# Kernel optimization log

Measured on AMD Instinct MI355X. Metric: run time of the kernel, lower is better.

## Reference

```python
import jax, jax.numpy as jnp
import numpy as np
jax.config.update("jax_enable_x64", True)
from jax.scipy.special import i0e

P = 256            # feature_num / contrast_dim
C = 1000           # num_classes
N = 512            # batch
TEMPERATURE = 1.0
ORDER = P // 2 - 1 # Bessel order nu = p/2 - 1


def _normalize(x, axis=-1, eps=1e-12):
    n = jnp.linalg.norm(x, axis=axis, keepdims=True)
    return x / jnp.maximum(n, eps)


def miller_recurrence(order, kappa):
    """Vectorized Miller backward recurrence for log I_order(k), log I_{order+1}(k).
    kappa: float64 array of any shape. Returns (log_I_order_scaled, log_I_order1_scaled)
    matching the torch reference (exponentially-scaled via i0e)."""
    ones = jnp.ones(kappa.shape, jnp.float64)
    zeros = jnp.zeros(kappa.shape, jnp.float64)
    init = (ones, zeros, zeros, zeros, zeros, zeros, zeros)
    iis = jnp.arange(2 * order, 0, -1)

    def step(carry, i):
        I_n, I_n1, scale, scale0, scale1, E0, E1 = carry
        coef = (2.0 * i) / kappa
        I_t = coef * I_n + I_n1
        ovf = jnp.any(jnp.isinf(I_t))  # global rescale trigger, as in torch
        logI = jnp.log(I_n)
        I_n1_r = I_n1 / I_n
        I_n_r = coef + I_n1_r          # recompute with I_n reset to 1
        I_n_new = jnp.where(ovf, I_n_r, I_t)
        I_n1_new = jnp.where(ovf, jnp.ones_like(I_n), I_n)
        scale = jnp.where(ovf, scale + logI, scale)
        scale0 = jnp.where(ovf & (i >= order), scale0 + logI, scale0)
        scale1 = jnp.where(ovf & (i >= order + 1), scale1 + logI, scale1)
        E0 = jnp.where(i == order, I_n1_new, E0)
        E1 = jnp.where(i == order + 1, I_n1_new, E1)
        return (I_n_new, I_n1_new, scale, scale0, scale1, E0, E1), None

    (I_n, _, scale, scale0, scale1, E0, E1), _ = jax.lax.scan(step, init, iis)
    live0 = jnp.log(i0e(kappa))
    e0 = live0 + jnp.log(E0) - jnp.log(I_n) + scale0 - scale
    e1 = live0 + jnp.log(E1) - jnp.log(I_n) + scale1 - scale
    return e0, e1


def setup_inputs() -> dict:
    key = jax.random.key(0)
    k1, k2, k3, k4 = jax.random.split(key, 4)
    features = jax.random.normal(k1, (N, P), dtype=jnp.float32)
    labels = jax.random.randint(k2, (N,), 0, C)
    real_span_mask = jax.random.randint(k3, (N,), 0, 2).astype(bool)
    Ave = (_normalize(jax.random.normal(k4, (C, P), dtype=jnp.float32), axis=1) * 0.9).astype(jnp.float32)
    Amount = jnp.zeros((C,), jnp.float32)
    return {"features": features, "labels": labels, "real_span_mask": real_span_mask,
            "Ave": Ave, "Amount": Amount}


def reference(features, labels, real_span_mask, Ave, Amount):
    feats = jax.lax.stop_gradient(features)
    # --- update_CV (masked rows contribute nothing, equivalent to boolean select) ---
    m = real_span_mask.astype(feats.dtype)                       # (N,)
    onehot = jax.nn.one_hot(labels, C, dtype=feats.dtype) * m[:, None]  # (N,C)
    counts = onehot.sum(0)                                       # (C,)
    feat_sum = jnp.einsum('nc,na->ca', onehot, feats)            # (C,A)
    denom = jnp.where(counts == 0, 1.0, counts)
    ave_CxA = feat_sum / denom[:, None]
    w = counts / (counts + Amount)
    w = jnp.where(jnp.isnan(w), 0.0, w)
    Ave_new = Ave * (1.0 - w[:, None]) + ave_CxA * w[:, None]    # (C,A)
    # --- update_kappa ---
    R = jnp.linalg.norm(Ave_new, axis=1)
    kappa = P * R / (1.0 - R ** 2)
    kappa = jnp.where((kappa > 1e5) | (kappa < 0), 1e5, kappa)   # f32 (C,)
    nu, _ = miller_recurrence(ORDER, kappa.astype(jnp.float64))
    logc = nu + kappa - (P / 2 - 1) * jnp.log(kappa + 1e-20)     # f64 (C,)
    # --- logits ---
    Ave_norm = _normalize(Ave_new, axis=1)
    temp = kappa[:, None] * Ave_norm                             # (C,A) f32
    t = temp[None, :, :] + features[:, None, :] / TEMPERATURE    # (N,C,A)
    kappa_new = jnp.linalg.norm(t, axis=2)                       # (N,C) f32
    nu_k, _ = miller_recurrence(ORDER, kappa_new.astype(jnp.float64))
    logits = (nu_k + kappa_new - (P / 2 - 1) * jnp.log(kappa_new + 1e-20)
              - logc[None, :]).astype(jnp.float32)
    return _normalize(logits, axis=1)
```

## Files before the change

kernel.cpp:

```cpp
#include <hip/hip_runtime.h>

static constexpr int NN = 512, CC = 1000, PP = 256, ORD = 127;

static constexpr size_t OFF_TEMPT  = 0;
static constexpr size_t OFF_KAPPA  = 1024000;
static constexpr size_t OFF_LOGC   = 1028096;
static constexpr size_t OFF_T2     = 1036288;
static constexpr size_t OFF_F2     = 1044480;
static constexpr size_t OFF_LOGITS = 1048576;
static constexpr size_t OFF_ACCUM  = OFF_LOGITS;
static constexpr size_t OFF_CNT    = OFF_LOGITS + 1024000;

__global__ __launch_bounds__(256) void k_scatter(
    const float* __restrict__ feats, const unsigned* __restrict__ A,
    const unsigned* __restrict__ B, float* __restrict__ accum,
    int* __restrict__ cnt, double* __restrict__ F2)
{
    __shared__ int s_fl[2];
    __shared__ double red4[4];
    const int n = blockIdx.x, tid = threadIdx.x;
    if (tid < 2) s_fl[tid] = 0;
    __syncthreads();
    int f0 = 0, f1 = 0;
    for (int w = tid; w < NN; w += 256) {
        if (A[w] > 1u) f0 = 1;
        if (B[w] > 1u) f1 = 1;
    }
    if (f0) atomicOr(&s_fl[0], 1);
    if (f1) atomicOr(&s_fl[1], 1);
    __syncthreads();
    const bool a_is_lab = s_fl[0] ? true : (s_fl[1] ? false : true);
    const unsigned* LAB = a_is_lab ? A : B;
    const unsigned* MSK = a_is_lab ? B : A;
    const int  lab = (int)LAB[n];
    const bool mk  = (MSK[n] != 0u);

    float v = feats[n * PP + tid];
    double ss = (double)v * (double)v;
    for (int off = 32; off > 0; off >>= 1) ss += __shfl_down(ss, off);
    if ((tid & 63) == 0) red4[tid >> 6] = ss;
    __syncthreads();
    if (tid == 0) F2[n] = red4[0] + red4[1] + red4[2] + red4[3];

    if (mk) {
        atomicAdd(&accum[lab * PP + tid], v);
        if (tid == 0) atomicAdd(&cnt[lab], 1);
    }
}

__global__ __launch_bounds__(256) void k_class(
    const float* __restrict__ accum, const int* __restrict__ cnt,
    const float* __restrict__ Ave, const float* __restrict__ Amount,
    float* __restrict__ tempT, float* __restrict__ kappa_out,
    double* __restrict__ T2, double* __restrict__ logc)
{
    __shared__ float  red4[4];
    __shared__ double redd[4];
    const int c = blockIdx.x, tid = threadIdx.x;
    float cntf   = (float)cnt[c];
    float amount = Amount[c];
    float w = cntf / (cntf + amount);
    if (isnan(w)) w = 0.f;
    float denom = (cntf == 0.f) ? 1.f : cntf;
    float ave = accum[c * PP + tid] / denom;
    float av_new = Ave[c * PP + tid] * (1.f - w) + ave * w;

    float ss = av_new * av_new;
    for (int off = 32; off > 0; off >>= 1) ss += __shfl_down(ss, off);
    if ((tid & 63) == 0) red4[tid >> 6] = ss;
    __syncthreads();
    float tot = red4[0] + red4[1] + red4[2] + red4[3];

    float R = sqrtf(tot);
    float kf = 256.0f * R / (1.0f - R * R);
    if (kf > 1e5f || kf < 0.0f) kf = 1e5f;
    float mu = av_new / fmaxf(R, 1e-12f);
    float tv = kf * mu;
    tempT[tid * CC + c] = tv;

    double ts = (double)tv * (double)tv;
    for (int off = 32; off > 0; off >>= 1) ts += __shfl_down(ts, off);
    if ((tid & 63) == 0) redd[tid >> 6] = ts;
    __syncthreads();

    if (tid == 0) {
        kappa_out[c] = kf;
        T2[c] = redd[0] + redd[1] + redd[2] + redd[3];
        float invf = 1.0f / kf;
        float In = 1.f, In1 = 0.f, i2 = 508.f;
        for (int it = 0; it < ORD; ++it) {
            float t = fmaf(i2 * invf, In, In1);
            In1 = In; In = t; i2 -= 2.f;
        }
        float E0 = In;
        for (int it = 0; it < ORD; ++it) {
            float t = fmaf(i2 * invf, In, In1);
            In1 = In; In = t; i2 -= 2.f;
        }
        float x = 0.125f * invf;
        float pser = x * (1.f + x * (4.5f + x * (37.5f + x * 459.375f)));
        float l1p = pser - 0.5f * pser * pser;
        float lr = logf(E0 / In);
        float lk = logf(kf);
        logc[c] = (double)(l1p + lr) - 0.9189385332046727
                  + (double)kf - 127.5 * (double)lk;
    }
}

__global__ __launch_bounds__(256) void k_main(
    const float* __restrict__ feats, const float* __restrict__ tempT,
    const double* __restrict__ T2, const double* __restrict__ F2,
    const double* __restrict__ logc, float* __restrict__ logits)
{
    __shared__ float f_s[4][PP];
    const int tid = threadIdx.x;
    const int n0  = blockIdx.y * 4;
    const int c   = blockIdx.x * 256 + tid;
    #pragma unroll
    for (int j = 0; j < 4; ++j)
        f_s[j][tid] = feats[(n0 + j) * PP + tid];
    __syncthreads();
    const bool act = (c < CC);

    float a0 = 0.f, a1 = 0.f, a2 = 0.f, a3 = 0.f;
    if (act) {
        #pragma unroll 4
        for (int a = 0; a < PP; ++a) {
            float tv = tempT[a * CC + c];
            a0 = fmaf(tv, f_s[0][a], a0);
            a1 = fmaf(tv, f_s[1][a], a1);
            a2 = fmaf(tv, f_s[2][a], a2);
            a3 = fmaf(tv, f_s[3][a], a3);
        }
    }
    float accs[4] = {a0, a1, a2, a3};
    double t2c = act ? T2[c] : 1.0e6;
    double kd[4];
    float kf[4], invf[4], In[4], In1[4], E0[4];
    #pragma unroll
    for (int j = 0; j < 4; ++j) {
        double kk = act ? (t2c + 2.0 * (double)accs[j] + F2[n0 + j]) : 1.0e6;
        kd[j]  = (double)(float)sqrt(kk);
        kf[j]  = (float)kd[j];
        invf[j] = 1.0f / kf[j];
        In[j] = 1.f; In1[j] = 0.f;
    }
    float i2 = 508.f;
    for (int it = 0; it < ORD; ++it) {
        #pragma unroll
        for (int j = 0; j < 4; ++j) {
            float t = fmaf(i2 * invf[j], In[j], In1[j]);
            In1[j] = In[j]; In[j] = t;
        }
        i2 -= 2.f;
    }
    #pragma unroll
    for (int j = 0; j < 4; ++j) E0[j] = In[j];
    for (int it = 0; it < ORD; ++it) {
        #pragma unroll
        for (int j = 0; j < 4; ++j) {
            float t = fmaf(i2 * invf[j], In[j], In1[j]);
            In1[j] = In[j]; In[j] = t;
        }
        i2 -= 2.f;
    }
    if (!act) return;
    double lgc = logc[c];
    #pragma unroll
    for (int j = 0; j < 4; ++j) {
        float x = 0.125f * invf[j];
        float pser = x * (1.f + x * (4.5f + x * (37.5f + x * 459.375f)));
        float l1p = pser - 0.5f * pser * pser;
        float lr = logf(E0[j] / In[j]);
        float lk = logf(kf[j]);
        double lg = (double)(l1p + lr) - 0.9189385332046727
                    + kd[j] - 127.5 * (double)lk - lgc;
        logits[(n0 + j) * CC + c] = (float)lg;
    }
}

__global__ __launch_bounds__(256) void k_norm(
    const float* __restrict__ logits, float* __restrict__ out)
{
    __shared__ double red4[4];
    const int n = blockIdx.x;
    const int tid = threadIdx.x;
    float v[4];
    double ss = 0.0;
    #pragma unroll
    for (int q = 0; q < 4; ++q) {
        int c = tid + q * 256;
        v[q] = (c < CC) ? logits[n * CC + c] : 0.f;
        ss += (double)v[q] * (double)v[q];
    }
    for (int off = 32; off > 0; off >>= 1) ss += __shfl_down(ss, off);
    if ((tid & 63) == 0) red4[tid >> 6] = ss;
    __syncthreads();
    double tot = red4[0] + red4[1] + red4[2] + red4[3];
    float inv = 1.0f / fmaxf((float)sqrt(tot), 1e-12f);
    #pragma unroll
    for (int q = 0; q < 4; ++q) {
        int c = tid + q * 256;
        if (c < CC) out[n * CC + c] = v[q] * inv;
    }
}

extern "C" void kernel_launch(void* const* d_in, const int* in_sizes, int n_in,
                              void* d_out, int out_size, void* d_ws, size_t ws_size,
                              hipStream_t stream) {
    int i_feat = -1, i_ave = -1, i_amt = -1, i5a = -1, i5b = -1;
    for (int i = 0; i < n_in; ++i) {
        int s = in_sizes[i];
        if      (s == NN * PP) i_feat = i;
        else if (s == CC * PP) i_ave  = i;
        else if (s == CC)      i_amt  = i;
        else if (s == NN)      { if (i5a < 0) i5a = i; else i5b = i; }
    }
    if (i_feat < 0 || i_ave < 0 || i_amt < 0 || i5a < 0 || i5b < 0) {
        i_feat = 0; i5a = 1; i5b = 2; i_ave = 3; i_amt = 4;
    }
    const float*    feats  = (const float*)d_in[i_feat];
    const unsigned* bufA   = (const unsigned*)d_in[i5a];
    const unsigned* bufB   = (const unsigned*)d_in[i5b];
    const float*    Ave    = (const float*)d_in[i_ave];
    const float*    Amount = (const float*)d_in[i_amt];

    char* ws = (char*)d_ws;
    float*  tempT  = (float*)(ws + OFF_TEMPT);
    float*  kappa  = (float*)(ws + OFF_KAPPA);
    double* logc   = (double*)(ws + OFF_LOGC);
    double* T2     = (double*)(ws + OFF_T2);
    double* F2     = (double*)(ws + OFF_F2);
    float*  logits = (float*)(ws + OFF_LOGITS);
    float*  accum  = (float*)(ws + OFF_ACCUM);
    int*    cnt    = (int*)(ws + OFF_CNT);
    float*  out    = (float*)d_out;

    hipMemsetAsync(ws + OFF_ACCUM, 0, (size_t)CC * PP * 4 + (size_t)CC * 4, stream);
    k_scatter<<<dim3(NN), dim3(256), 0, stream>>>(feats, bufA, bufB, accum, cnt, F2);
    k_class<<<dim3(CC), dim3(256), 0, stream>>>(accum, cnt, Ave, Amount,
                                                tempT, kappa, T2, logc);
    k_main<<<dim3(4, NN / 4), dim3(256), 0, stream>>>(feats, tempT, T2, F2,
                                                      logc, logits);
    k_norm<<<dim3(NN), dim3(256), 0, stream>>>(logits, out);
}
```

Measured before the change: 108.9 us.

## Fuse all stages into one cooperative kernel with grid syncs and gather-based class sums

Result: slower. 193.5 us (+77.6%).

```diff
diff --git a/kernel.cpp b/kernel.cpp
--- a/kernel.cpp
+++ b/kernel.cpp
@@ -1,207 +1,219 @@
 #include <hip/hip_runtime.h>
+#include <hip/hip_cooperative_groups.h>
+namespace cg = cooperative_groups;
 
 static constexpr int NN = 512, CC = 1000, PP = 256, ORD = 127;
 
 static constexpr size_t OFF_TEMPT  = 0;
-static constexpr size_t OFF_KAPPA  = 1024000;
-static constexpr size_t OFF_LOGC   = 1028096;
-static constexpr size_t OFF_T2     = 1036288;
-static constexpr size_t OFF_F2     = 1044480;
+static constexpr size_t OFF_LOGC   = 1024000;
+static constexpr size_t OFF_T2     = 1032000;
+static constexpr size_t OFF_F2     = 1040000;
 static constexpr size_t OFF_LOGITS = 1048576;
-static constexpr size_t OFF_ACCUM  = OFF_LOGITS;
-static constexpr size_t OFF_CNT    = OFF_LOGITS + 1024000;
-
-__global__ __launch_bounds__(256) void k_scatter(
+
+__global__ __launch_bounds__(256) void k_fused(
     const float* __restrict__ feats, const unsigned* __restrict__ A,
-    const unsigned* __restrict__ B, float* __restrict__ accum,
-    int* __restrict__ cnt, double* __restrict__ F2)
+    const unsigned* __restrict__ B, const float* __restrict__ Ave,
+    const float* __restrict__ Amount, float* __restrict__ tempT,
+    double* __restrict__ logcv, double* __restrict__ T2,
+    double* __restrict__ F2, float* __restrict__ logits,
+    float* __restrict__ out)
 {
-    __shared__ int s_fl[2];
-    __shared__ double red4[4];
-    const int n = blockIdx.x, tid = threadIdx.x;
+    cg::grid_group grid = cg::this_grid();
+    const int b = blockIdx.x, tid = threadIdx.x;
+
+    __shared__ float  f_s[4][PP];
+    __shared__ float  red4[4];
+    __shared__ double redd[4];
+    __shared__ int    s_list[64];
+    __shared__ int    s_lcnt;
+    __shared__ int    s_fl[2];
+    __shared__ float  s_kf[2];
+
     if (tid < 2) s_fl[tid] = 0;
     __syncthreads();
-    int f0 = 0, f1 = 0;
-    for (int w = tid; w < NN; w += 256) {
-        if (A[w] > 1u) f0 = 1;
-        if (B[w] > 1u) f1 = 1;
-    }
-    if (f0) atomicOr(&s_fl[0], 1);
-    if (f1) atomicOr(&s_fl[1], 1);
+    {
+        int f0 = 0, f1 = 0;
+        for (int w = tid; w < NN; w += 256) {
+            if (A[w] > 1u) f0 = 1;
+            if (B[w] > 1u) f1 = 1;
+        }
+        if (f0) atomicOr(&s_fl[0], 1);
+        if (f1) atomicOr(&s_fl[1], 1);
+    }
     __syncthreads();
     const bool a_is_lab = s_fl[0] ? true : (s_fl[1] ? false : true);
     const unsigned* LAB = a_is_lab ? A : B;
     const unsigned* MSK = a_is_lab ? B : A;
-    const int  lab = (int)LAB[n];
-    const bool mk  = (MSK[n] != 0u);
-
-    float v = feats[n * PP + tid];
-    double ss = (double)v * (double)v;
-    for (int off = 32; off > 0; off >>= 1) ss += __shfl_down(ss, off);
-    if ((tid & 63) == 0) red4[tid >> 6] = ss;
-    __syncthreads();
-    if (tid == 0) F2[n] = red4[0] + red4[1] + red4[2] + red4[3];
-
-    if (mk) {
-        atomicAdd(&accum[lab * PP + tid], v);
-        if (tid == 0) atomicAdd(&cnt[lab], 1);
-    }
-}
-
-__global__ __launch_bounds__(256) void k_class(
-    const float* __restrict__ accum, const int* __restrict__ cnt,
-    const float* __restrict__ Ave, const float* __restrict__ Amount,
-    float* __restrict__ tempT, float* __restrict__ kappa_out,
-    double* __restrict__ T2, double* __restrict__ logc)
-{
-    __shared__ float  red4[4];
-    __shared__ double redd[4];
-    const int c = blockIdx.x, tid = threadIdx.x;
-    float cntf   = (float)cnt[c];
-    float amount = Amount[c];
-    float w = cntf / (cntf + amount);
-    if (isnan(w)) w = 0.f;
-    float denom = (cntf == 0.f) ? 1.f : cntf;
-    float ave = accum[c * PP + tid] / denom;
-    float av_new = Ave[c * PP + tid] * (1.f - w) + ave * w;
-
-    float ss = av_new * av_new;
-    for (int off = 32; off > 0; off >>= 1) ss += __shfl_down(ss, off);
-    if ((tid & 63) == 0) red4[tid >> 6] = ss;
-    __syncthreads();
-    float tot = red4[0] + red4[1] + red4[2] + red4[3];
-
-    float R = sqrtf(tot);
-    float kf = 256.0f * R / (1.0f - R * R);
-    if (kf > 1e5f || kf < 0.0f) kf = 1e5f;
-    float mu = av_new / fmaxf(R, 1e-12f);
-    float tv = kf * mu;
-    tempT[tid * CC + c] = tv;
-
-    double ts = (double)tv * (double)tv;
-    for (int off = 32; off > 0; off >>= 1) ts += __shfl_down(ts, off);
-    if ((tid & 63) == 0) redd[tid >> 6] = ts;
-    __syncthreads();
-
-    if (tid == 0) {
-        kappa_out[c] = kf;
-        T2[c] = redd[0] + redd[1] + redd[2] + redd[3];
+
+    {
+        float v = feats[b * PP + tid];
+        double ss = (double)v * (double)v;
+        for (int off = 32; off > 0; off >>= 1) ss += __shfl_down(ss, off);
+        if ((tid & 63) == 0) redd[tid >> 6] = ss;
+        __syncthreads();
+        if (tid == 0) F2[b] = redd[0] + redd[1] + redd[2] + redd[3];
+        __syncthreads();
+    }
+
+    for (int q = 0; q < 2; ++q) {
+        int c = b + q * 512;
+        if (c < CC) {
+            if (tid == 0) s_lcnt = 0;
+            __syncthreads();
+            for (int n = tid; n < NN; n += 256) {
+                if (MSK[n] != 0u && (int)LAB[n] == c) {
+                    int i = atomicAdd(&s_lcnt, 1);
+                    if (i < 64) s_list[i] = n;
+                }
+            }
+            __syncthreads();
+            int lc = s_lcnt < 64 ? s_lcnt : 64;
+            float sum = 0.f;
+            for (int i = 0; i < lc; ++i) sum += feats[s_list[i] * PP + tid];
+            float cntf = (float)s_lcnt;
+            float amount = Amount[c];
+            float w = cntf / (cntf + amount);
+            if (isnan(w)) w = 0.f;
+            float denom = (cntf == 0.f) ? 1.f : cntf;
+            float ave = sum / denom;
+            float av_new = Ave[c * PP + tid] * (1.f - w) + ave * w;
+
+            float ss = av_new * av_new;
+            for (int off = 32; off > 0; off >>= 1) ss += __shfl_down(ss, off);
+            if ((tid & 63) == 0) red4[tid >> 6] = ss;
+            __syncthreads();
+            float tot = red4[0] + red4[1] + red4[2] + red4[3];
+
+            float R = sqrtf(tot);
+            float kf = 256.0f * R / (1.0f - R * R);
+            if (kf > 1e5f || kf < 0.0f) kf = 1e5f;
+            float mu = av_new / fmaxf(R, 1e-12f);
+            float tv = kf * mu;
+            tempT[tid * CC + c] = tv;
+
+            double ts = (double)tv * (double)tv;
+            for (int off = 32; off > 0; off >>= 1) ts += __shfl_down(ts, off);
+            if ((tid & 63) == 0) redd[tid >> 6] = ts;
+            __syncthreads();
+            if (tid == 0) {
+                T2[c] = redd[0] + redd[1] + redd[2] + redd[3];
+                s_kf[q] = kf;
+            }
+            __syncthreads();
+        }
+    }
+    if (tid < 2 && (b + tid * 512) < CC) {
+        int c = b + tid * 512;
+        float kf = s_kf[tid];
         float invf = 1.0f / kf;
         float In = 1.f, In1 = 0.f, i2 = 508.f;
         for (int it = 0; it < ORD; ++it) {
-            float t = fmaf(i2 * invf, In, In1);
-            In1 = In; In = t; i2 -= 2.f;
+            float t = fmaf(i2 * invf, In, In1); In1 = In; In = t; i2 -= 2.f;
         }
         float E0 = In;
         for (int it = 0; it < ORD; ++it) {
-            float t = fmaf(i2 * invf, In, In1);
-            In1 = In; In = t; i2 -= 2.f;
+            float t = fmaf(i2 * invf, In, In1); In1 = In; In = t; i2 -= 2.f;
         }
         float x = 0.125f * invf;
         float pser = x * (1.f + x * (4.5f + x * (37.5f + x * 459.375f)));
         float l1p = pser - 0.5f * pser * pser;
         float lr = logf(E0 / In);
         float lk = logf(kf);
-        logc[c] = (double)(l1p + lr) - 0.9189385332046727
-                  + (double)kf - 127.5 * (double)lk;
-    }
-}
-
-__global__ __launch_bounds__(256) void k_main(
-    const float* __restrict__ feats, const float* __restrict__ tempT,
-    const double* __restrict__ T2, const double* __restrict__ F2,
-    const double* __restrict__ logc, float* __restrict__ logits)
-{
-    __shared__ float f_s[4][PP];
-    const int tid = threadIdx.x;
-    const int n0  = blockIdx.y * 4;
-    const int c   = blockIdx.x * 256 + tid;
-    #pragma unroll
-    for (int j = 0; j < 4; ++j)
-        f_s[j][tid] = feats[(n0 + j) * PP + tid];
-    __syncthreads();
-    const bool act = (c < CC);
-
-    float a0 = 0.f, a1 = 0.f, a2 = 0.f, a3 = 0.f;
-    if (act) {
-        #pragma unroll 4
-        for (int a = 0; a < PP; ++a) {
-            float tv = tempT[a * CC + c];
-            a0 = fmaf(tv, f_s[0][a], a0);
-            a1 = fmaf(tv, f_s[1][a], a1);
-            a2 = fmaf(tv, f_s[2][a], a2);
-            a3 = fmaf(tv, f_s[3][a], a3);
-        }
-    }
-    float accs[4] = {a0, a1, a2, a3};
-    double t2c = act ? T2[c] : 1.0e6;
-    double kd[4];
-    float kf[4], invf[4], In[4], In1[4], E0[4];
-    #pragma unroll
-    for (int j = 0; j < 4; ++j) {
-        double kk = act ? (t2c + 2.0 * (double)accs[j] + F2[n0 + j]) : 1.0e6;
-        kd[j]  = (double)(float)sqrt(kk);
-        kf[j]  = (float)kd[j];
-        invf[j] = 1.0f / kf[j];
-        In[j] = 1.f; In1[j] = 0.f;
-    }
-    float i2 = 508.f;
-    for (int it = 0; it < ORD; ++it) {
+        logcv[c] = (double)(l1p + lr) - 0.9189385332046727
+                   + (double)kf - 127.5 * (double)lk;
+    }
+
+    grid.sync();
+
+    {
+        const int ct = b & 3, nt = b >> 2;
+        const int c  = ct * 256 + tid;
+        const int n0 = nt * 4;
+        #pragma unroll
+        for (int j = 0; j < 4; ++j)
+            f_s[j][tid] = feats[(n0 + j) * PP + tid];
+        __syncthreads();
+        const bool act = (c < CC);
+
+        float a0 = 0.f, a1 = 0.f, a2 = 0.f, a3 = 0.f;
+        if (act) {
+            #pragma unroll 4
+            for (int a = 0; a < PP; ++a) {
+                float tv = tempT[a * CC + c];
+                a0 = fmaf(tv, f_s[0][a], a0);
+                a1 = fmaf(tv, f_s[1][a], a1);
+                a2 = fmaf(tv, f_s[2][a], a2);
+                a3 = fmaf(tv, f_s[3][a], a3);
+            }
+        }
+        float accs[4] = {a0, a1, a2, a3};
+        double t2c = act ? T2[c] : 1.0e6;
+        double kd[4];
+        float kf[4], invf[4], In[4], In1[4], E0[4];
         #pragma unroll
         for (int j = 0; j < 4; ++j) {
-            float t = fmaf(i2 * invf[j], In[j], In1[j]);
-            In1[j] = In[j]; In[j] = t;
-        }
-        i2 -= 2.f;
-    }
-    #pragma unroll
-    for (int j = 0; j < 4; ++j) E0[j] = In[j];
-    for (int it = 0; it < ORD; ++it) {
-        #pragma unroll
-        for (int j = 0; j < 4; ++j) {
-            float t = fmaf(i2 * invf[j], In[j], In1[j]);
-            In1[j] = In[j]; In[j] = t;
-        }
-        i2 -= 2.f;
-    }
-    if (!act) return;
-    double lgc = logc[c];
-    #pragma unroll
-    for (int j = 0; j < 4; ++j) {
-        float x = 0.125f * invf[j];
-        float pser = x * (1.f + x * (4.5f + x * (37.5f + x * 459.375f)));
-        float l1p = pser - 0.5f * pser * pser;
-        float lr = logf(E0[j] / In[j]);
-        float lk = logf(kf[j]);
-        double lg = (double)(l1p + lr) - 0.9189385332046727
-                    + kd[j] - 127.5 * (double)lk - lgc;
-        logits[(n0 + j) * CC + c] = (float)lg;
-    }
-}
-
-__global__ __launch_bounds__(256) void k_norm(
-    const float* __restrict__ logits, float* __restrict__ out)
-{
-    __shared__ double red4[4];
-    const int n = blockIdx.x;
-    const int tid = threadIdx.x;
-    float v[4];
-    double ss = 0.0;
-    #pragma unroll
-    for (int q = 0; q < 4; ++q) {
-        int c = tid + q * 256;
-        v[q] = (c < CC) ? logits[n * CC + c] : 0.f;
-        ss += (double)v[q] * (double)v[q];
-    }
-    for (int off = 32; off > 0; off >>= 1) ss += __shfl_down(ss, off);
-    if ((tid & 63) == 0) red4[tid >> 6] = ss;
-    __syncthreads();
-    double tot = red4[0] + red4[1] + red4[2] + red4[3];
-    float inv = 1.0f / fmaxf((float)sqrt(tot), 1e-12f);
-    #pragma unroll
-    for (int q = 0; q < 4; ++q) {
-        int c = tid + q * 256;
-        if (c < CC) out[n * CC + c] = v[q] * inv;
+            double kk = act ? (t2c + 2.0 * (double)accs[j] + F2[n0 + j]) : 1.0e6;
+            kd[j]  = (double)(float)sqrt(kk);
+            kf[j]  = (float)kd[j];
+            invf[j] = 1.0f / kf[j];
+            In[j] = 1.f; In1[j] = 0.f;
+        }
+        float i2 = 508.f;
+        for (int it = 0; it < ORD; ++it) {
+            #pragma unroll
+            for (int j = 0; j < 4; ++j) {
+                float t = fmaf(i2 * invf[j], In[j], In1[j]);
+                In1[j] = In[j]; In[j] = t;
+            }
+            i2 -= 2.f;
+        }
+        #pragma unroll
+        for (int j = 0; j < 4; ++j) E0[j] = In[j];
+        for (int it = 0; it < ORD; ++it) {
+            #pragma unroll
+            for (int j = 0; j < 4; ++j) {
+                float t = fmaf(i2 * invf[j], In[j], In1[j]);
+                In1[j] = In[j]; In[j] = t;
+            }
+            i2 -= 2.f;
+        }
+        if (act) {
+            double lgc = logcv[c];
+            #pragma unroll
+            for (int j = 0; j < 4; ++j) {
+                float x = 0.125f * invf[j];
+                float pser = x * (1.f + x * (4.5f + x * (37.5f + x * 459.375f)));
+                float l1p = pser - 0.5f * pser * pser;
+                float lr = logf(E0[j] / In[j]);
+                float lk = logf(kf[j]);
+                double lg = (double)(l1p + lr) - 0.9189385332046727
+                            + kd[j] - 127.5 * (double)lk - lgc;
+                logits[(n0 + j) * CC + c] = (float)lg;
+            }
+        }
+    }
+
+    grid.sync();
+
+    {
+        float v[4];
+        double ss = 0.0;
+        #pragma unroll
+        for (int q = 0; q < 4; ++q) {
+            int c = tid + q * 256;
+            v[q] = (c < CC) ? logits[b * CC + c] : 0.f;
+            ss += (double)v[q] * (double)v[q];
+        }
+        for (int off = 32; off > 0; off >>= 1) ss += __shfl_down(ss, off);
+        if ((tid & 63) == 0) redd[tid >> 6] = ss;
+        __syncthreads();
+        double tot = redd[0] + redd[1] + redd[2] + redd[3];
+        float inv = 1.0f / fmaxf((float)sqrt(tot), 1e-12f);
+        #pragma unroll
+        for (int q = 0; q < 4; ++q) {
+            int c = tid + q * 256;
+            if (c < CC) out[b * CC + c] = v[q] * inv;
+        }
     }
 }
 
@@ -227,20 +239,15 @@
 
     char* ws = (char*)d_ws;
     float*  tempT  = (float*)(ws + OFF_TEMPT);
-    float*  kappa  = (float*)(ws + OFF_KAPPA);
-    double* logc   = (double*)(ws + OFF_LOGC);
+    double* logcv  = (double*)(ws + OFF_LOGC);
     double* T2     = (double*)(ws + OFF_T2);
     double* F2     = (double*)(ws + OFF_F2);
     float*  logits = (float*)(ws + OFF_LOGITS);
-    float*  accum  = (float*)(ws + OFF_ACCUM);
-    int*    cnt    = (int*)(ws + OFF_CNT);
     float*  out    = (float*)d_out;
 
-    hipMemsetAsync(ws + OFF_ACCUM, 0, (size_t)CC * PP * 4 + (size_t)CC * 4, stream);
-    k_scatter<<<dim3(NN), dim3(256), 0, stream>>>(feats, bufA, bufB, accum, cnt, F2);
-    k_class<<<dim3(CC), dim3(256), 0, stream>>>(accum, cnt, Ave, Amount,
-                                                tempT, kappa, T2, logc);
-    k_main<<<dim3(4, NN / 4), dim3(256), 0, stream>>>(feats, tempT, T2, F2,
-                                                      logc, logits);
-    k_norm<<<dim3(NN), dim3(256), 0, stream>>>(logits, out);
+    void* args[] = { (void*)&feats, (void*)&bufA, (void*)&bufB, (void*)&Ave,
+                     (void*)&Amount, (void*)&tempT, (void*)&logcv, (void*)&T2,
+                     (void*)&F2, (void*)&logits, (void*)&out };
+    hipLaunchCooperativeKernel(reinterpret_cast<void*>(k_fused),
+                               dim3(NN), dim3(256), args, 0, stream);
 }
```
